# Kernel optimization log

Measured on AMD Instinct MI355X. Metric: run time of the kernel, lower is better.

The kernel has to match this reference:

```python
import math
import jax, jax.numpy as jnp
import numpy as np

G = 128        # graphs per batch
N0 = 512       # nodes per graph
H = 256        # hidden size
E = 524288     # edges (avg degree 8), intra-graph
RATIO = 0.8


def setup_inputs() -> dict:
    key = jax.random.key(0)
    ks = jax.random.split(key, 16)
    # intra-graph edges: E//G edges per graph
    eg = jnp.arange(E, dtype=jnp.int32) // (E // G)
    src = eg * N0 + jax.random.randint(ks[0], (E,), 0, N0, dtype=jnp.int32)
    dst = eg * N0 + jax.random.randint(ks[1], (E,), 0, N0, dtype=jnp.int32)
    s = 1.0 / math.sqrt(H)
    return {
        "x": jax.random.normal(ks[2], (G * N0, H), jnp.float32),
        "edge_src": src,
        "edge_dst": dst,
        "W_in": jax.random.normal(ks[3], (H, H), jnp.float32) * s,
        "b_in": jnp.zeros((H,), jnp.float32),
        "W_h0": jax.random.normal(ks[4], (H, H), jnp.float32) * s,
        "b_h0": jnp.zeros((H,), jnp.float32),
        "W_h1": jax.random.normal(ks[5], (H, H), jnp.float32) * s,
        "b_h1": jnp.zeros((H,), jnp.float32),
        "p_in": jax.random.normal(ks[6], (H,), jnp.float32),
        "p_h0": jax.random.normal(ks[7], (H,), jnp.float32),
        "p_h1": jax.random.normal(ks[8], (H,), jnp.float32),
        "att_w": jax.random.normal(ks[9], (H,), jnp.float32) * s,
        "att_b": jnp.zeros((1,), jnp.float32),
    }


def gcn_conv(x, W, b, src, dst, emask, num_nodes):
    # PyG GCNConv: lin -> sym-normalized propagate (with self loops, weight 1) -> bias
    h = x @ W
    deg = jax.ops.segment_sum(emask, dst, num_segments=num_nodes) + 1.0  # +1 self loop
    dis = jax.lax.rsqrt(deg)
    coef = dis[src] * dis[dst] * emask                    # [E]
    agg = jax.ops.segment_sum(h[src] * coef[:, None], dst, num_segments=num_nodes)
    agg = agg + h * (dis * dis)[:, None]                  # self-loop message
    return agg + b


def topk_pool(x, p, src, dst, emask, n_cur):
    # PyG TopKPooling: score = tanh(x.p/|p|), keep top ceil(ratio*n) per graph,
    # x' = x[perm]*score[perm], edges filtered to kept nodes and remapped.
    k = int(math.ceil(RATIO * n_cur))
    score = jnp.tanh((x @ p) / jnp.linalg.norm(p))        # [G*n_cur]
    _, idx = jax.lax.top_k(score.reshape(G, n_cur), k)    # [G,k]
    perm = (idx + (jnp.arange(G, dtype=idx.dtype) * n_cur)[:, None]).reshape(-1)
    x_new = x[perm] * score[perm][:, None]                # [G*k,H]
    mapping = jnp.full((G * n_cur,), -1, jnp.int32).at[perm].set(
        jnp.arange(G * k, dtype=jnp.int32))
    ns, nd = mapping[src], mapping[dst]
    valid = (ns >= 0) & (nd >= 0) & (emask > 0)
    return (x_new, jnp.where(valid, ns, 0), jnp.where(valid, nd, 0),
            valid.astype(x.dtype), k)


def att_pool(x, att_w, att_b, k):
    # GlobalAttention: per-graph softmax gate, weighted sum
    gate = (x @ att_w + att_b[0]).reshape(G, k)
    att = jax.nn.softmax(gate, axis=1)
    return jnp.einsum('gk,gkh->gh', att, x.reshape(G, k, H))


def reference(x, edge_src, edge_dst, W_in, b_in, W_h0, b_h0, W_h1, b_h1,
              p_in, p_h0, p_h1, att_w, att_b):
    src, dst = edge_src, edge_dst
    emask = jnp.ones((E,), x.dtype)
    n_cur = N0
    h = jax.nn.relu(gcn_conv(x, W_in, b_in, src, dst, emask, G * n_cur))
    h, src, dst, emask, n_cur = topk_pool(h, p_in, src, dst, emask, n_cur)
    out = att_pool(h, att_w, att_b, n_cur)
    for (W, b, p) in ((W_h0, b_h0, p_h0), (W_h1, b_h1, p_h1)):
        h = jax.nn.relu(gcn_conv(h, W, b, src, dst, emask, G * n_cur))
        h, src, dst, emask, n_cur = topk_pool(h, p, src, dst, emask, n_cur)
        out = out + att_pool(h, att_w, att_b, n_cur)
    return out  # [G, H]
```

## Files before the change

### kernel.cpp

```cpp
#include <hip/hip_runtime.h>
#include <cmath>

#define G_ 128
#define N0_ 512
#define H_ 256
#define E_ 524288
#define NODES0 (G_*N0_)

typedef _Float16 v8h __attribute__((ext_vector_type(8)));
typedef _Float16 v4h __attribute__((ext_vector_type(4)));
typedef float v4f __attribute__((ext_vector_type(4)));

#define TSTRIDE 72
#define TILEHW (128*TSTRIDE)

__device__ __forceinline__ void async_copy16(void* lds, const void* g) {
  __builtin_amdgcn_global_load_lds(
      (const __attribute__((address_space(1))) void*)g,
      (__attribute__((address_space(3))) void*)lds, 16, 0, 0);
}

__device__ __forceinline__ float4 f4fma(float4 a, float s, float4 acc) {
  acc.x = fmaf(a.x, s, acc.x); acc.y = fmaf(a.y, s, acc.y);
  acc.z = fmaf(a.z, s, acc.z); acc.w = fmaf(a.w, s, acc.w);
  return acc;
}

__device__ __forceinline__ float block_reduce_sum(float v, volatile float* red) {
  #pragma unroll
  for (int off = 32; off > 0; off >>= 1) v += __shfl_down(v, off);
  int lane = threadIdx.x & 63, wid = threadIdx.x >> 6;
  __syncthreads();
  if (lane == 0) red[wid] = v;
  __syncthreads();
  return red[0] + red[1] + red[2] + red[3];
}

__global__ __launch_bounds__(256) void pnorm_kernel(const float* __restrict__ p0,
                                                    const float* __restrict__ p1,
                                                    const float* __restrict__ p2,
                                                    float* __restrict__ pinv) {
  __shared__ float red[4];
  const float* p = (blockIdx.x == 0) ? p0 : (blockIdx.x == 1 ? p1 : p2);
  float v = p[threadIdx.x];
  float s = block_reduce_sum(v * v, red);
  if (threadIdx.x == 0) pinv[blockIdx.x] = 1.0f / sqrtf(s);
}

__global__ void init_kernel(int* __restrict__ cum, int* __restrict__ orig_of,
                            int* __restrict__ cnt, int n) {
  int v = blockIdx.x * 256 + threadIdx.x;
  if (v < n) { cum[v] = v; orig_of[v] = v; cnt[v] = 0; }
}

__global__ __launch_bounds__(256) void wconv_kernel(const float* __restrict__ W0,
                                                    const float* __restrict__ W1,
                                                    const float* __restrict__ W2,
                                                    _Float16* __restrict__ img) {
  int l = blockIdx.x >> 4;
  const float* W = (l == 0) ? W0 : (l == 1 ? W1 : W2);
  int bn = (blockIdx.x >> 3) & 1, kt = blockIdx.x & 7;
  int t = threadIdx.x;
  int n = t & 127, kh = t >> 7;
  int k0 = kt * 32 + kh * 16;
  _Float16* row = img + (size_t)l * 16 * TILEHW + ((size_t)(bn * 8 + kt) * 128 + n) * TSTRIDE;
  #pragma unroll
  for (int s = 0; s < 2; ++s) {
    v8h hv, lv;
    #pragma unroll
    for (int j = 0; j < 8; ++j) {
      float a = W[(size_t)(k0 + s * 8 + j) * 256 + bn * 128 + n];
      _Float16 h = (_Float16)a;
      hv[j] = h;
      lv[j] = (_Float16)(a - (float)h);
    }
    *(v8h*)&row[kh * 16 + s * 8] = hv;
    *(v8h*)&row[32 + kh * 16 + s * 8] = lv;
  }
}

__global__ void count0_kernel(const int* __restrict__ edst, int* __restrict__ cnt) {
  int e = blockIdx.x * 256 + threadIdx.x;
  if (e < E_) atomicAdd(&cnt[edst[e]], 1);
}

__global__ __launch_bounds__(256) void scan1_kernel(const int* __restrict__ cnt,
                                                    int* __restrict__ row0,
                                                    int* __restrict__ bsum,
                                                    float* __restrict__ dis,
                                                    int* __restrict__ cursor, int n) {
  __shared__ int sdata[256];
  int base = blockIdx.x * 1024;
  int t = threadIdx.x;
  int v[4]; int s = 0;
  #pragma unroll
  for (int i = 0; i < 4; ++i) {
    int idx = base + t * 4 + i;
    v[i] = (idx < n) ? cnt[idx] : 0;
    s += v[i];
    if (idx < n) {
      dis[idx] = 1.0f / sqrtf((float)v[i] + 1.0f);
      cursor[idx] = 0;
    }
  }
  sdata[t] = s;
  __syncthreads();
  for (int off = 1; off < 256; off <<= 1) {
    int x = (t >= off) ? sdata[t - off] : 0;
    __syncthreads();
    sdata[t] += x;
    __syncthreads();
  }
  int excl = sdata[t] - s;
  if (t == 255) bsum[blockIdx.x] = sdata[255];
  #pragma unroll
  for (int i = 0; i < 4; ++i) {
    int idx = base + t * 4 + i;
    if (idx < n) { row0[idx] = excl; excl += v[i]; }
  }
}

__global__ __launch_bounds__(256) void scan2_kernel(int* __restrict__ bsum,
                                                    int* __restrict__ row0, int nb, int n) {
  __shared__ int sdata[256];
  int t = threadIdx.x;
  int v = (t < nb) ? bsum[t] : 0;
  sdata[t] = v;
  __syncthreads();
  for (int off = 1; off < 256; off <<= 1) {
    int x = (t >= off) ? sdata[t - off] : 0;
    __syncthreads();
    sdata[t] += x;
    __syncthreads();
  }
  if (t < nb) bsum[t] = sdata[t] - v;
  if (t == 255) row0[n] = sdata[255];
}

__global__ void fill0_kernel(const int* __restrict__ esrc, const int* __restrict__ edst,
                             const int* __restrict__ row0, const int* __restrict__ bsum,
                             int* __restrict__ cursor, const float* __restrict__ dis,
                             int* __restrict__ csr0, int* __restrict__ csr_dst,
                             float* __restrict__ cf0) {
  int e = blockIdx.x * 256 + threadIdx.x;
  if (e >= E_) return;
  int d = edst[e], s = esrc[e];
  int pos = atomicAdd(&cursor[d], 1);
  int idx = row0[d] + bsum[d >> 10] + pos;
  csr0[idx] = s;
  csr_dst[idx] = d;
  cf0[idx] = dis[s] * dis[d];
}

__global__ void deg_kernel(const int* __restrict__ orig_of, const int* __restrict__ row0,
                           const int* __restrict__ bsum, const int* __restrict__ csr0,
                           const int* __restrict__ cum, float* __restrict__ dis, int nodes) {
  int v = blockIdx.x * 256 + threadIdx.x;
  if (v >= nodes) return;
  int o = orig_of[v];
  int rs = row0[o] + bsum[o >> 10];
  int o1 = o + 1;
  int re = row0[o1] + ((o1 < NODES0) ? bsum[o1 >> 10] : 0);
  int c = 0;
  for (int j = rs; j < re; ++j) c += (cum[csr0[j]] >= 0) ? 1 : 0;
  dis[v] = rsqrtf((float)c + 1.0f);
}

__global__ void remap_kernel(const int* __restrict__ csr0, const int* __restrict__ csr_dst,
                             const int* __restrict__ cum, const float* __restrict__ dis,
                             int* __restrict__ src_l, float* __restrict__ cf_l) {
  int j = blockIdx.x * 256 + threadIdx.x;
  if (j >= E_) return;
  int md = cum[csr_dst[j]];
  if (md < 0) return;
  int ms = cum[csr0[j]];
  src_l[j] = (ms >= 0) ? ms : 0;
  cf_l[j] = (ms >= 0) ? dis[ms] * dis[md] : 0.0f;
}

__global__ __launch_bounds__(256) void gemm_f16x3_kernel(const float* __restrict__ A,
                                                         const int* __restrict__ perm,
                                                         const float* __restrict__ score,
                                                         const _Float16* __restrict__ Wimg,
                                                         float* __restrict__ C) {
  __shared__ _Float16 As[TILEHW];
  __shared__ _Float16 Ws[TILEHW];
  const int tid = threadIdx.x;
  const int bm = blockIdx.x >> 1;
  const int bn = blockIdx.x & 1;
  const int lane = tid & 63, wid = tid >> 6;
  const int wm = wid >> 1, wn = wid & 1;
  const int l15 = lane & 15, kg = lane >> 4;

  v4f acc[4][4];
  #pragma unroll
  for (int i = 0; i < 4; ++i)
    #pragma unroll
    for (int j = 0; j < 4; ++j) acc[i][j] = (v4f){0.f, 0.f, 0.f, 0.f};

  int arow[4], acc4[4];
  const float* aptr[4];
  float ascale[4];
  #pragma unroll
  for (int i = 0; i < 4; ++i) {
    int c = tid + 256 * i;
    arow[i] = c >> 3;
    acc4[i] = c & 7;
    int R = bm * 128 + arow[i];
    int pr = perm ? perm[R] : R;
    ascale[i] = perm ? score[pr] : 1.0f;
    aptr[i] = A + (size_t)pr * 256 + acc4[i] * 4;
  }
  const _Float16* wtile0 = Wimg + (size_t)bn * 8 * TILEHW;

  float4 pa[4];
  #pragma unroll
  for (int i = 0; i < 4; ++i) pa[i] = *(const float4*)(aptr[i] + 0);

  for (int kt = 0; kt < 8; ++kt) {
    {
      const _Float16* wt = wtile0 + (size_t)kt * TILEHW;
      for (int cb = wid; cb < 18; cb += 4)
        async_copy16(&Ws[cb * 512], wt + (size_t)cb * 512 + lane * 8);
    }
    #pragma unroll
    for (int i = 0; i < 4; ++i) {
      float av[4] = {pa[i].x * ascale[i], pa[i].y * ascale[i],
                     pa[i].z * ascale[i], pa[i].w * ascale[i]};
      v4h hv, lv;
      #pragma unroll
      for (int j = 0; j < 4; ++j) {
        _Float16 h = (_Float16)av[j];
        hv[j] = h;
        lv[j] = (_Float16)(av[j] - (float)h);
      }
      _Float16* dst = &As[arow[i] * TSTRIDE + acc4[i] * 4];
      *(v4h*)(dst) = hv;
      *(v4h*)(dst + 32) = lv;
    }
    __syncthreads();

    if (kt < 7) {
      #pragma unroll
      for (int i = 0; i < 4; ++i)
        pa[i] = *(const float4*)(aptr[i] + (kt + 1) * 32);
    }

    v8h ah[4], bh[4], al[4], bl[4];
    #pragma unroll
    for (int i = 0; i < 4; ++i)
      ah[i] = *(const v8h*)&As[(wm * 64 + i * 16 + l15) * TSTRIDE + kg * 8];
    #pragma unroll
    for (int j = 0; j < 4; ++j)
      bh[j] = *(const v8h*)&Ws[(wn * 64 + j * 16 + l15) * TSTRIDE + kg * 8];
    #pragma unroll
    for (int i = 0; i < 4; ++i)
      #pragma unroll
      for (int j = 0; j < 4; ++j)
        acc[i][j] = __builtin_amdgcn_mfma_f32_16x16x32_f16(ah[i], bh[j], acc[i][j], 0, 0, 0);
    #pragma unroll
    for (int i = 0; i < 4; ++i)
      al[i] = *(const v8h*)&As[(wm * 64 + i * 16 + l15) * TSTRIDE + 32 + kg * 8];
    #pragma unroll
    for (int i = 0; i < 4; ++i)
      #pragma unroll
      for (int j = 0; j < 4; ++j)
        acc[i][j] = __builtin_amdgcn_mfma_f32_16x16x32_f16(al[i], bh[j], acc[i][j], 0, 0, 0);
    #pragma unroll
    for (int j = 0; j < 4; ++j)
      bl[j] = *(const v8h*)&Ws[(wn * 64 + j * 16 + l15) * TSTRIDE + 32 + kg * 8];
    #pragma unroll
    for (int i = 0; i < 4; ++i)
      #pragma unroll
      for (int j = 0; j < 4; ++j)
        acc[i][j] = __builtin_amdgcn_mfma_f32_16x16x32_f16(ah[i], bl[j], acc[i][j], 0, 0, 0);
    __syncthreads();
  }

  #pragma unroll
  for (int i = 0; i < 4; ++i) {
    #pragma unroll
    for (int j = 0; j < 4; ++j) {
      #pragma unroll
      for (int r = 0; r < 4; ++r) {
        int row = bm * 128 + wm * 64 + i * 16 + kg * 4 + r;
        int col = bn * 128 + wn * 64 + j * 16 + l15;
        C[(size_t)row * 256 + col] = acc[i][j][r];
      }
    }
  }
}

__global__ __launch_bounds__(256) void agg_score_kernel(
    const float4* __restrict__ hlin4, const float* __restrict__ dis,
    const float4* __restrict__ bias4,
    const int* __restrict__ orig_of, const int* __restrict__ row0,
    const int* __restrict__ bsum,
    const int* __restrict__ src_arr, const float* __restrict__ cf_arr,
    const float4* __restrict__ p4, const float* __restrict__ pinvp,
    float4* __restrict__ hout4, float* __restrict__ score, int q) {
  int blk = (blockIdx.x & 7) * q + (blockIdx.x >> 3);
  int wave = threadIdx.x >> 6, lane = threadIdx.x & 63;
  int v = blk * 4 + wave;
  float dv = dis[v];
  float self = dv * dv;
  float4 h = hlin4[(size_t)v * 64 + lane];
  float4 acc = make_float4(h.x * self, h.y * self, h.z * self, h.w * self);
  int o = orig_of[v];
  int rs = row0[o] + bsum[o >> 10];
  int o1 = o + 1;
  int re = row0[o1] + ((o1 < NODES0) ? bsum[o1 >> 10] : 0);
  int j = rs;
  for (; j + 8 <= re; j += 8) {
    int s[8]; float c[8]; float4 hh[8];
    #pragma unroll
    for (int u = 0; u < 8; ++u) { s[u] = src_arr[j + u]; c[u] = cf_arr[j + u]; }
    #pragma unroll
    for (int u = 0; u < 8; ++u) hh[u] = hlin4[(size_t)s[u] * 64 + lane];
    #pragma unroll
    for (int u = 0; u < 8; ++u) acc = f4fma(hh[u], c[u], acc);
  }
  if (j + 4 <= re) {
    int s[4]; float c[4]; float4 hh[4];
    #pragma unroll
    for (int u = 0; u < 4; ++u) { s[u] = src_arr[j + u]; c[u] = cf_arr[j + u]; }
    #pragma unroll
    for (int u = 0; u < 4; ++u) hh[u] = hlin4[(size_t)s[u] * 64 + lane];
    #pragma unroll
    for (int u = 0; u < 4; ++u) acc = f4fma(hh[u], c[u], acc);
    j += 4;
  }
  for (; j < re; ++j) {
    acc = f4fma(hlin4[(size_t)src_arr[j] * 64 + lane], cf_arr[j], acc);
  }
  float4 b = bias4[lane];
  acc.x = fmaxf(acc.x + b.x, 0.0f); acc.y = fmaxf(acc.y + b.y, 0.0f);
  acc.z = fmaxf(acc.z + b.z, 0.0f); acc.w = fmaxf(acc.w + b.w, 0.0f);
  hout4[(size_t)v * 64 + lane] = acc;
  float4 pv = p4[lane];
  float s = acc.x * pv.x + acc.y * pv.y + acc.z * pv.z + acc.w * pv.w;
  #pragma unroll
  for (int off = 32; off > 0; off >>= 1) s += __shfl_down(s, off);
  if (lane == 0) score[v] = tanhf(s * pinvp[0]);
}

__global__ __launch_bounds__(256) void topk_kernel(const float* __restrict__ score, int n, int k,
                                                   int* __restrict__ cum,
                                                   const int* __restrict__ orig_prev,
                                                   int* __restrict__ orig_new,
                                                   int* __restrict__ perm) {
  __shared__ float key[512];
  __shared__ int kid[512];
  __shared__ int newmap[512];
  int g = blockIdx.x, t = threadIdx.x;
  for (int i = t; i < 512; i += 256) {
    key[i] = (i < n) ? score[(size_t)g * n + i] : -INFINITY;
    kid[i] = i;
    if (i < n) newmap[i] = -1;
  }
  __syncthreads();
  for (int kk = 2; kk <= 512; kk <<= 1) {
    for (int j = kk >> 1; j > 0; j >>= 1) {
      #pragma unroll
      for (int half = 0; half < 2; ++half) {
        int i = t + half * 256;
        int ixj = i ^ j;
        if (ixj > i) {
          float ka = key[i]; int ia = kid[i];
          float kb = key[ixj]; int ib = kid[ixj];
          bool b_first = (kb > ka) || (kb == ka && ib < ia);
          bool sw = ((i & kk) == 0) ? b_first : !b_first;
          if (sw) { key[i] = kb; kid[i] = ib; key[ixj] = ka; kid[ixj] = ia; }
        }
      }
      __syncthreads();
    }
  }
  for (int i = t; i < k; i += 256) {
    int local = kid[i];
    perm[g * k + i] = g * n + local;
    newmap[local] = g * k + i;
    orig_new[g * k + i] = orig_prev[g * n + local];
  }
  __syncthreads();
  #pragma unroll
  for (int u = 0; u < N0_ / 256; ++u) {
    int v = g * N0_ + u * 256 + t;
    int c = cum[v];
    if (c >= 0) cum[v] = newmap[c - g * n];
  }
}

__global__ __launch_bounds__(512) void pool_kernel(
    const float4* __restrict__ h4, const float* __restrict__ score,
    const int* __restrict__ perm,
    const float4* __restrict__ attw4, const float* __restrict__ attb,
    float* __restrict__ out, int k, int add) {
  __shared__ float wmax[8], wsum[8];
  __shared__ float4 waccs[8][64];
  int g = blockIdx.x, t = threadIdx.x;
  int wave = t >> 6, lane = t & 63;
  float4 aw = attw4[lane];
  float ab = attb[0];

  float m = -INFINITY, ssum = 0.0f;
  float4 acc = make_float4(0.f, 0.f, 0.f, 0.f);
  for (int i = wave; i < k; i += 8) {
    int s = perm[g * k + i];
    float sc = score[s];
    float4 hv = h4[(size_t)s * 64 + lane];
    float4 val = make_float4(hv.x * sc, hv.y * sc, hv.z * sc, hv.w * sc);
    float gd = val.x * aw.x + val.y * aw.y + val.z * aw.z + val.w * aw.w;
    #pragma unroll
    for (int off = 32; off > 0; off >>= 1) gd += __shfl_xor(gd, off);
    float gi = gd + ab;
    float mnew = fmaxf(m, gi);
    float f = __expf(m - mnew);
    float e = __expf(gi - mnew);
    acc.x = acc.x * f + val.x * e; acc.y = acc.y * f + val.y * e;
    acc.z = acc.z * f + val.z * e; acc.w = acc.w * f + val.w * e;
    ssum = ssum * f + e;
    m = mnew;
  }
  if (lane == 0) { wmax[wave] = m; wsum[wave] = ssum; }
  waccs[wave][lane] = acc;
  __syncthreads();
  if (wave == 0) {
    float mstar = wmax[0];
    #pragma unroll
    for (int w = 1; w < 8; ++w) mstar = fmaxf(mstar, wmax[w]);
    float stot = 0.0f;
    float4 a = make_float4(0.f, 0.f, 0.f, 0.f);
    #pragma unroll
    for (int w = 0; w < 8; ++w) {
      float sc = __expf(wmax[w] - mstar);
      stot += wsum[w] * sc;
      float4 wa = waccs[w][lane];
      a.x += wa.x * sc; a.y += wa.y * sc; a.z += wa.z * sc; a.w += wa.w * sc;
    }
    float inv = 1.0f / stot;
    a.x *= inv; a.y *= inv; a.z *= inv; a.w *= inv;
    float4* o4 = (float4*)out + (size_t)g * 64 + lane;
    if (add) {
      float4 prev = *o4;
      a.x += prev.x; a.y += prev.y; a.z += prev.z; a.w += prev.w;
    }
    *o4 = a;
  }
}

extern "C" void kernel_launch(void* const* d_in, const int* in_sizes, int n_in,
                              void* d_out, int out_size, void* d_ws, size_t ws_size,
                              hipStream_t stream) {
  const float* x    = (const float*)d_in[0];
  const int*   esrc = (const int*)d_in[1];
  const int*   edst = (const int*)d_in[2];
  const float* Wl[3] = {(const float*)d_in[3], (const float*)d_in[5], (const float*)d_in[7]};
  const float* bl[3] = {(const float*)d_in[4], (const float*)d_in[6], (const float*)d_in[8]};
  const float* pl[3] = {(const float*)d_in[9], (const float*)d_in[10], (const float*)d_in[11]};
  const float* attw = (const float*)d_in[12];
  const float* attb = (const float*)d_in[13];
  float* out = (float*)d_out;

  char* w = (char*)d_ws;
  auto carve = [&](size_t bytes) { char* p = w; w += (bytes + 255) & ~(size_t)255; return p; };
  float* bufA    = (float*)carve((size_t)NODES0 * H_ * 4);
  float* bufB    = (float*)carve((size_t)NODES0 * H_ * 4);
  int*   csr0    = (int*)  carve((size_t)E_ * 4);
  int*   csr_dst = (int*)  carve((size_t)E_ * 4);
  float* cf0     = (float*)carve((size_t)E_ * 4);
  int*   src_l   = (int*)  carve((size_t)E_ * 4);
  float* cf_l    = (float*)carve((size_t)E_ * 4);
  int*   cnt     = (int*)  carve((size_t)NODES0 * 4);
  int*   row0    = (int*)  carve((size_t)(NODES0 + 1) * 4);
  int*   cursor  = (int*)  carve((size_t)NODES0 * 4);
  float* dis     = (float*)carve((size_t)NODES0 * 4);
  float* score   = (float*)carve((size_t)NODES0 * 4);
  int*   cum_map = (int*)  carve((size_t)NODES0 * 4);
  int*   origA   = (int*)  carve((size_t)NODES0 * 4);
  int*   origB   = (int*)  carve((size_t)NODES0 * 4);
  int*   perm    = (int*)  carve((size_t)NODES0 * 4);
  int*   bsum    = (int*)  carve(256 * 4);
  float* pinv    = (float*)carve(16);
  _Float16* Wimg = (_Float16*)carve((size_t)3 * 16 * TILEHW * 2);
  (void)ws_size; (void)in_sizes; (void)n_in; (void)out_size;

  pnorm_kernel<<<3, 256, 0, stream>>>(pl[0], pl[1], pl[2], pinv);
  init_kernel<<<NODES0 / 256, 256, 0, stream>>>(cum_map, origA, cnt, NODES0);
  wconv_kernel<<<48, 256, 0, stream>>>(Wl[0], Wl[1], Wl[2], Wimg);

  count0_kernel<<<E_ / 256, 256, 0, stream>>>(edst, cnt);
  int nb0 = (NODES0 + 1023) / 1024;
  scan1_kernel<<<nb0, 256, 0, stream>>>(cnt, row0, bsum, dis, cursor, NODES0);
  scan2_kernel<<<1, 256, 0, stream>>>(bsum, row0, nb0, NODES0);
  fill0_kernel<<<E_ / 256, 256, 0, stream>>>(esrc, edst, row0, bsum, cursor, dis,
                                             csr0, csr_dst, cf0);

  int n_cur = N0_;
  int* origs[2] = {origA, origB};
  for (int l = 0; l < 3; ++l) {
    int nodes = G_ * n_cur;
    int* orig_cur = origs[l & 1];
    int* orig_nxt = origs[(l & 1) ^ 1];

    if (l > 0) {
      deg_kernel<<<(nodes + 255) / 256, 256, 0, stream>>>(orig_cur, row0, bsum, csr0,
                                                          cum_map, dis, nodes);
      remap_kernel<<<E_ / 256, 256, 0, stream>>>(csr0, csr_dst, cum_map, dis, src_l, cf_l);
    }

    gemm_f16x3_kernel<<<(nodes / 128) * 2, 256, 0, stream>>>(
        (l == 0) ? x : bufB, (l == 0) ? nullptr : perm, score,
        Wimg + (size_t)l * 16 * TILEHW, bufA);

    int agg_blocks = nodes / 4;
    agg_score_kernel<<<agg_blocks, 256, 0, stream>>>(
        (const float4*)bufA, dis, (const float4*)bl[l], orig_cur, row0, bsum,
        (l == 0) ? csr0 : src_l, (l == 0) ? cf0 : cf_l,
        (const float4*)pl[l], pinv + l, (float4*)bufB, score, agg_blocks / 8);

    int kk = (int)std::ceil(0.8 * (double)n_cur);
    topk_kernel<<<G_, 256, 0, stream>>>(score, n_cur, kk, cum_map, orig_cur, orig_nxt, perm);

    pool_kernel<<<G_, 512, 0, stream>>>(
        (const float4*)bufB, score, perm, (const float4*)attw, attb, out, kk, l > 0 ? 1 : 0);

    n_cur = kk;
  }
}
```

Baseline: 411.2 us.

## Stage per-graph feature slices in LDS for GCN aggregation, split score reduction

The aggregation kernel now runs one 1024-thread block per graph per pair of 64-column slices. It stages the graph's node features for each slice into LDS with async global-to-LDS copies, then gathers neighbours from LDS instead of global memory, relying on edges being intra-graph. Per-slice partial score dots go to a new buffer, and the topk kernel sums them and applies tanh. This cuts scattered global gathers but uses only 256 blocks with 128KB LDS each, which limits occupancy and parallelism. Invalid edges now point at the destination node so LDS indices stay in range.

```diff
diff --git a/kernel.cpp b/kernel.cpp
--- a/kernel.cpp
+++ b/kernel.cpp
@@ -174,7 +174,7 @@
   int md = cum[csr_dst[j]];
   if (md < 0) return;
   int ms = cum[csr0[j]];
-  src_l[j] = (ms >= 0) ? ms : 0;
+  src_l[j] = (ms >= 0) ? ms : md;
   cf_l[j] = (ms >= 0) ? dis[ms] * dis[md] : 0.0f;
 }
 
@@ -291,60 +291,66 @@
   }
 }
 
-__global__ __launch_bounds__(256) void agg_score_kernel(
-    const float4* __restrict__ hlin4, const float* __restrict__ dis,
-    const float4* __restrict__ bias4,
+__global__ __launch_bounds__(1024) void agg_score_kernel(
+    const float* __restrict__ hlin, const float* __restrict__ dis,
+    const float* __restrict__ bias,
     const int* __restrict__ orig_of, const int* __restrict__ row0,
     const int* __restrict__ bsum,
     const int* __restrict__ src_arr, const float* __restrict__ cf_arr,
-    const float4* __restrict__ p4, const float* __restrict__ pinvp,
-    float4* __restrict__ hout4, float* __restrict__ score, int q) {
-  int blk = (blockIdx.x & 7) * q + (blockIdx.x >> 3);
-  int wave = threadIdx.x >> 6, lane = threadIdx.x & 63;
-  int v = blk * 4 + wave;
-  float dv = dis[v];
-  float self = dv * dv;
-  float4 h = hlin4[(size_t)v * 64 + lane];
-  float4 acc = make_float4(h.x * self, h.y * self, h.z * self, h.w * self);
-  int o = orig_of[v];
-  int rs = row0[o] + bsum[o >> 10];
-  int o1 = o + 1;
-  int re = row0[o1] + ((o1 < NODES0) ? bsum[o1 >> 10] : 0);
-  int j = rs;
-  for (; j + 8 <= re; j += 8) {
-    int s[8]; float c[8]; float4 hh[8];
-    #pragma unroll
-    for (int u = 0; u < 8; ++u) { s[u] = src_arr[j + u]; c[u] = cf_arr[j + u]; }
-    #pragma unroll
-    for (int u = 0; u < 8; ++u) hh[u] = hlin4[(size_t)s[u] * 64 + lane];
-    #pragma unroll
-    for (int u = 0; u < 8; ++u) acc = f4fma(hh[u], c[u], acc);
-  }
-  if (j + 4 <= re) {
-    int s[4]; float c[4]; float4 hh[4];
-    #pragma unroll
-    for (int u = 0; u < 4; ++u) { s[u] = src_arr[j + u]; c[u] = cf_arr[j + u]; }
-    #pragma unroll
-    for (int u = 0; u < 4; ++u) hh[u] = hlin4[(size_t)s[u] * 64 + lane];
-    #pragma unroll
-    for (int u = 0; u < 4; ++u) acc = f4fma(hh[u], c[u], acc);
-    j += 4;
-  }
-  for (; j < re; ++j) {
-    acc = f4fma(hlin4[(size_t)src_arr[j] * 64 + lane], cf_arr[j], acc);
-  }
-  float4 b = bias4[lane];
-  acc.x = fmaxf(acc.x + b.x, 0.0f); acc.y = fmaxf(acc.y + b.y, 0.0f);
-  acc.z = fmaxf(acc.z + b.z, 0.0f); acc.w = fmaxf(acc.w + b.w, 0.0f);
-  hout4[(size_t)v * 64 + lane] = acc;
-  float4 pv = p4[lane];
-  float s = acc.x * pv.x + acc.y * pv.y + acc.z * pv.z + acc.w * pv.w;
-  #pragma unroll
-  for (int off = 32; off > 0; off >>= 1) s += __shfl_down(s, off);
-  if (lane == 0) score[v] = tanhf(s * pinvp[0]);
-}
-
-__global__ __launch_bounds__(256) void topk_kernel(const float* __restrict__ score, int n, int k,
+    const float* __restrict__ p,
+    float* __restrict__ hout, float* __restrict__ scorepart, int n) {
+  __shared__ float sh[512 * 64];
+  int g = blockIdx.x >> 1;
+  int s0 = (blockIdx.x & 1) * 2;
+  int t = threadIdx.x, wave = t >> 6, lane = t & 63;
+  const int nodebase = g * n;
+
+  for (int s = s0; s < s0 + 2; ++s) {
+    for (int r4 = wave * 4; r4 < n; r4 += 64) {
+      const float* src = hlin + (size_t)(nodebase + r4 + (lane >> 4)) * 256
+                              + s * 64 + (lane & 15) * 4;
+      async_copy16(&sh[r4 * 64], src);
+    }
+    __syncthreads();
+
+    float bb = bias[s * 64 + lane];
+    float pp = p[s * 64 + lane];
+
+    for (int vl = wave; vl < n; vl += 16) {
+      int v = nodebase + vl;
+      float dv = dis[v];
+      float acc = sh[vl * 64 + lane] * (dv * dv);
+      int o = orig_of[v];
+      int rs = row0[o] + bsum[o >> 10];
+      int o1 = o + 1;
+      int re = row0[o1] + ((o1 < NODES0) ? bsum[o1 >> 10] : 0);
+      int j = rs;
+      for (; j + 8 <= re; j += 8) {
+        int sl[8]; float cf[8];
+        #pragma unroll
+        for (int u = 0; u < 8; ++u) { sl[u] = src_arr[j + u] - nodebase; cf[u] = cf_arr[j + u]; }
+        float hv[8];
+        #pragma unroll
+        for (int u = 0; u < 8; ++u) hv[u] = sh[sl[u] * 64 + lane];
+        #pragma unroll
+        for (int u = 0; u < 8; ++u) acc = fmaf(hv[u], cf[u], acc);
+      }
+      for (; j < re; ++j)
+        acc = fmaf(sh[(src_arr[j] - nodebase) * 64 + lane], cf_arr[j], acc);
+      acc = fmaxf(acc + bb, 0.0f);
+      hout[(size_t)v * 256 + s * 64 + lane] = acc;
+      float sdot = acc * pp;
+      #pragma unroll
+      for (int off = 32; off > 0; off >>= 1) sdot += __shfl_down(sdot, off);
+      if (lane == 0) scorepart[(size_t)v * 4 + s] = sdot;
+    }
+    __syncthreads();
+  }
+}
+
+__global__ __launch_bounds__(256) void topk_kernel(const float* __restrict__ scorepart,
+                                                   const float* __restrict__ pinvp,
+                                                   float* __restrict__ score, int n, int k,
                                                    int* __restrict__ cum,
                                                    const int* __restrict__ orig_prev,
                                                    int* __restrict__ orig_new,
@@ -353,10 +359,18 @@
   __shared__ int kid[512];
   __shared__ int newmap[512];
   int g = blockIdx.x, t = threadIdx.x;
+  float pinv = pinvp[0];
   for (int i = t; i < 512; i += 256) {
-    key[i] = (i < n) ? score[(size_t)g * n + i] : -INFINITY;
+    float sc = -INFINITY;
+    if (i < n) {
+      const float* sp = scorepart + (size_t)(g * n + i) * 4;
+      float tot = ((sp[0] + sp[1]) + sp[2]) + sp[3];
+      sc = tanhf(tot * pinv);
+      score[g * n + i] = sc;
+      newmap[i] = -1;
+    }
+    key[i] = sc;
     kid[i] = i;
-    if (i < n) newmap[i] = -1;
   }
   __syncthreads();
   for (int kk = 2; kk <= 512; kk <<= 1) {
@@ -476,6 +490,7 @@
   int*   cursor  = (int*)  carve((size_t)NODES0 * 4);
   float* dis     = (float*)carve((size_t)NODES0 * 4);
   float* score   = (float*)carve((size_t)NODES0 * 4);
+  float* spart   = (float*)carve((size_t)NODES0 * 4 * 4);
   int*   cum_map = (int*)  carve((size_t)NODES0 * 4);
   int*   origA   = (int*)  carve((size_t)NODES0 * 4);
   int*   origB   = (int*)  carve((size_t)NODES0 * 4);
@@ -513,14 +528,14 @@
         (l == 0) ? x : bufB, (l == 0) ? nullptr : perm, score,
         Wimg + (size_t)l * 16 * TILEHW, bufA);
 
-    int agg_blocks = nodes / 4;
-    agg_score_kernel<<<agg_blocks, 256, 0, stream>>>(
-        (const float4*)bufA, dis, (const float4*)bl[l], orig_cur, row0, bsum,
+    agg_score_kernel<<<G_ * 2, 1024, 0, stream>>>(
+        bufA, dis, bl[l], orig_cur, row0, bsum,
         (l == 0) ? csr0 : src_l, (l == 0) ? cf0 : cf_l,
-        (const float4*)pl[l], pinv + l, (float4*)bufB, score, agg_blocks / 8);
+        pl[l], bufB, spart, n_cur);
 
     int kk = (int)std::ceil(0.8 * (double)n_cur);
-    topk_kernel<<<G_, 256, 0, stream>>>(score, n_cur, kk, cum_map, orig_cur, orig_nxt, perm);
+    topk_kernel<<<G_, 256, 0, stream>>>(spart, pinv + l, score, n_cur, kk,
+                                        cum_map, orig_cur, orig_nxt, perm);
 
     pool_kernel<<<G_, 512, 0, stream>>>(
         (const float4*)bufB, score, perm, (const float4*)attw, attb, out, kk, l > 0 ? 1 : 0);
```

Measured after the change: 602.2 us. 1.46x slower.

## Fuse top-k with attention pooling and pack edge src/coef into int2

Applied to the files above, without the earlier changes.

Merges the top-k sort kernel and the attention pooling kernel into one 512-thread kernel per graph. The pooling step now reads sorted scores and indices straight from shared memory instead of indirecting through perm and the global score array. Edge source indices and normalization coefficients are interleaved into int2 pairs, so the aggregation loop does one 8-byte load per edge instead of two scattered 4-byte loads. The sorted scores are also written to a compact sscore array so the GEMM gather reads them contiguously. Invalid remapped edges now point at the destination node with zero coefficient rather than node 0.

```diff
diff --git a/kernel.cpp b/kernel.cpp
--- a/kernel.cpp
+++ b/kernel.cpp
@@ -141,7 +141,7 @@
                              const int* __restrict__ row0, const int* __restrict__ bsum,
                              int* __restrict__ cursor, const float* __restrict__ dis,
                              int* __restrict__ csr0, int* __restrict__ csr_dst,
-                             float* __restrict__ cf0) {
+                             int2* __restrict__ pair0) {
   int e = blockIdx.x * 256 + threadIdx.x;
   if (e >= E_) return;
   int d = edst[e], s = esrc[e];
@@ -149,7 +149,7 @@
   int idx = row0[d] + bsum[d >> 10] + pos;
   csr0[idx] = s;
   csr_dst[idx] = d;
-  cf0[idx] = dis[s] * dis[d];
+  pair0[idx] = make_int2(s, __float_as_int(dis[s] * dis[d]));
 }
 
 __global__ void deg_kernel(const int* __restrict__ orig_of, const int* __restrict__ row0,
@@ -168,19 +168,19 @@
 
 __global__ void remap_kernel(const int* __restrict__ csr0, const int* __restrict__ csr_dst,
                              const int* __restrict__ cum, const float* __restrict__ dis,
-                             int* __restrict__ src_l, float* __restrict__ cf_l) {
+                             int2* __restrict__ pair_l) {
   int j = blockIdx.x * 256 + threadIdx.x;
   if (j >= E_) return;
   int md = cum[csr_dst[j]];
   if (md < 0) return;
   int ms = cum[csr0[j]];
-  src_l[j] = (ms >= 0) ? ms : 0;
-  cf_l[j] = (ms >= 0) ? dis[ms] * dis[md] : 0.0f;
+  pair_l[j] = make_int2((ms >= 0) ? ms : md,
+                        __float_as_int((ms >= 0) ? dis[ms] * dis[md] : 0.0f));
 }
 
 __global__ __launch_bounds__(256) void gemm_f16x3_kernel(const float* __restrict__ A,
                                                          const int* __restrict__ perm,
-                                                         const float* __restrict__ score,
+                                                         const float* __restrict__ sscore,
                                                          const _Float16* __restrict__ Wimg,
                                                          float* __restrict__ C) {
   __shared__ _Float16 As[TILEHW];
@@ -208,7 +208,7 @@
     acc4[i] = c & 7;
     int R = bm * 128 + arow[i];
     int pr = perm ? perm[R] : R;
-    ascale[i] = perm ? score[pr] : 1.0f;
+    ascale[i] = perm ? sscore[R] : 1.0f;
     aptr[i] = A + (size_t)pr * 256 + acc4[i] * 4;
   }
   const _Float16* wtile0 = Wimg + (size_t)bn * 8 * TILEHW;
@@ -296,7 +296,7 @@
     const float4* __restrict__ bias4,
     const int* __restrict__ orig_of, const int* __restrict__ row0,
     const int* __restrict__ bsum,
-    const int* __restrict__ src_arr, const float* __restrict__ cf_arr,
+    const int2* __restrict__ edge,
     const float4* __restrict__ p4, const float* __restrict__ pinvp,
     float4* __restrict__ hout4, float* __restrict__ score, int q) {
   int blk = (blockIdx.x & 7) * q + (blockIdx.x >> 3);
@@ -314,7 +314,10 @@
   for (; j + 8 <= re; j += 8) {
     int s[8]; float c[8]; float4 hh[8];
     #pragma unroll
-    for (int u = 0; u < 8; ++u) { s[u] = src_arr[j + u]; c[u] = cf_arr[j + u]; }
+    for (int u = 0; u < 8; ++u) {
+      int2 e = edge[j + u];
+      s[u] = e.x; c[u] = __int_as_float(e.y);
+    }
     #pragma unroll
     for (int u = 0; u < 8; ++u) hh[u] = hlin4[(size_t)s[u] * 64 + lane];
     #pragma unroll
@@ -323,7 +326,10 @@
   if (j + 4 <= re) {
     int s[4]; float c[4]; float4 hh[4];
     #pragma unroll
-    for (int u = 0; u < 4; ++u) { s[u] = src_arr[j + u]; c[u] = cf_arr[j + u]; }
+    for (int u = 0; u < 4; ++u) {
+      int2 e = edge[j + u];
+      s[u] = e.x; c[u] = __int_as_float(e.y);
+    }
     #pragma unroll
     for (int u = 0; u < 4; ++u) hh[u] = hlin4[(size_t)s[u] * 64 + lane];
     #pragma unroll
@@ -331,7 +337,8 @@
     j += 4;
   }
   for (; j < re; ++j) {
-    acc = f4fma(hlin4[(size_t)src_arr[j] * 64 + lane], cf_arr[j], acc);
+    int2 e = edge[j];
+    acc = f4fma(hlin4[(size_t)e.x * 64 + lane], __int_as_float(e.y), acc);
   }
   float4 b = bias4[lane];
   acc.x = fmaxf(acc.x + b.x, 0.0f); acc.y = fmaxf(acc.y + b.y, 0.0f);
@@ -344,71 +351,59 @@
   if (lane == 0) score[v] = tanhf(s * pinvp[0]);
 }
 
-__global__ __launch_bounds__(256) void topk_kernel(const float* __restrict__ score, int n, int k,
-                                                   int* __restrict__ cum,
-                                                   const int* __restrict__ orig_prev,
-                                                   int* __restrict__ orig_new,
-                                                   int* __restrict__ perm) {
+__global__ __launch_bounds__(512) void topk_pool_kernel(
+    const float* __restrict__ score, int n, int k,
+    int* __restrict__ cum, const int* __restrict__ orig_prev,
+    int* __restrict__ orig_new, int* __restrict__ perm, float* __restrict__ sscore,
+    const float4* __restrict__ h4, const float4* __restrict__ attw4,
+    const float* __restrict__ attb, float* __restrict__ out, int add) {
   __shared__ float key[512];
   __shared__ int kid[512];
   __shared__ int newmap[512];
-  int g = blockIdx.x, t = threadIdx.x;
-  for (int i = t; i < 512; i += 256) {
-    key[i] = (i < n) ? score[(size_t)g * n + i] : -INFINITY;
-    kid[i] = i;
-    if (i < n) newmap[i] = -1;
-  }
-  __syncthreads();
-  for (int kk = 2; kk <= 512; kk <<= 1) {
-    for (int j = kk >> 1; j > 0; j >>= 1) {
-      #pragma unroll
-      for (int half = 0; half < 2; ++half) {
-        int i = t + half * 256;
-        int ixj = i ^ j;
-        if (ixj > i) {
-          float ka = key[i]; int ia = kid[i];
-          float kb = key[ixj]; int ib = kid[ixj];
-          bool b_first = (kb > ka) || (kb == ka && ib < ia);
-          bool sw = ((i & kk) == 0) ? b_first : !b_first;
-          if (sw) { key[i] = kb; kid[i] = ib; key[ixj] = ka; kid[ixj] = ia; }
-        }
-      }
-      __syncthreads();
-    }
-  }
-  for (int i = t; i < k; i += 256) {
-    int local = kid[i];
-    perm[g * k + i] = g * n + local;
-    newmap[local] = g * k + i;
-    orig_new[g * k + i] = orig_prev[g * n + local];
-  }
-  __syncthreads();
-  #pragma unroll
-  for (int u = 0; u < N0_ / 256; ++u) {
-    int v = g * N0_ + u * 256 + t;
-    int c = cum[v];
-    if (c >= 0) cum[v] = newmap[c - g * n];
-  }
-}
-
-__global__ __launch_bounds__(512) void pool_kernel(
-    const float4* __restrict__ h4, const float* __restrict__ score,
-    const int* __restrict__ perm,
-    const float4* __restrict__ attw4, const float* __restrict__ attb,
-    float* __restrict__ out, int k, int add) {
   __shared__ float wmax[8], wsum[8];
   __shared__ float4 waccs[8][64];
   int g = blockIdx.x, t = threadIdx.x;
+
+  key[t] = (t < n) ? score[(size_t)g * n + t] : -INFINITY;
+  kid[t] = t;
+  if (t < n) newmap[t] = -1;
+  __syncthreads();
+  for (int kk = 2; kk <= 512; kk <<= 1) {
+    for (int j = kk >> 1; j > 0; j >>= 1) {
+      int i = t, ixj = i ^ j;
+      if (ixj > i) {
+        float ka = key[i]; int ia = kid[i];
+        float kb = key[ixj]; int ib = kid[ixj];
+        bool b_first = (kb > ka) || (kb == ka && ib < ia);
+        bool sw = ((i & kk) == 0) ? b_first : !b_first;
+        if (sw) { key[i] = kb; kid[i] = ib; key[ixj] = ka; kid[ixj] = ia; }
+      }
+      __syncthreads();
+    }
+  }
+  if (t < k) {
+    int local = kid[t];
+    perm[g * k + t] = g * n + local;
+    newmap[local] = g * k + t;
+    orig_new[g * k + t] = orig_prev[g * n + local];
+    sscore[g * k + t] = key[t];
+  }
+  __syncthreads();
+  {
+    int v = g * N0_ + t;
+    int c = cum[v];
+    if (c >= 0) cum[v] = newmap[c - g * n];
+  }
+
   int wave = t >> 6, lane = t & 63;
   float4 aw = attw4[lane];
   float ab = attb[0];
-
   float m = -INFINITY, ssum = 0.0f;
   float4 acc = make_float4(0.f, 0.f, 0.f, 0.f);
   for (int i = wave; i < k; i += 8) {
-    int s = perm[g * k + i];
-    float sc = score[s];
-    float4 hv = h4[(size_t)s * 64 + lane];
+    int node = g * n + kid[i];
+    float sc = key[i];
+    float4 hv = h4[(size_t)node * 64 + lane];
     float4 val = make_float4(hv.x * sc, hv.y * sc, hv.z * sc, hv.w * sc);
     float gd = val.x * aw.x + val.y * aw.y + val.z * aw.z + val.w * aw.w;
     #pragma unroll
@@ -468,14 +463,14 @@
   float* bufB    = (float*)carve((size_t)NODES0 * H_ * 4);
   int*   csr0    = (int*)  carve((size_t)E_ * 4);
   int*   csr_dst = (int*)  carve((size_t)E_ * 4);
-  float* cf0     = (float*)carve((size_t)E_ * 4);
-  int*   src_l   = (int*)  carve((size_t)E_ * 4);
-  float* cf_l    = (float*)carve((size_t)E_ * 4);
+  int2*  pair0   = (int2*) carve((size_t)E_ * 8);
+  int2*  pair_l  = (int2*) carve((size_t)E_ * 8);
   int*   cnt     = (int*)  carve((size_t)NODES0 * 4);
   int*   row0    = (int*)  carve((size_t)(NODES0 + 1) * 4);
   int*   cursor  = (int*)  carve((size_t)NODES0 * 4);
   float* dis     = (float*)carve((size_t)NODES0 * 4);
   float* score   = (float*)carve((size_t)NODES0 * 4);
+  float* sscore  = (float*)carve((size_t)NODES0 * 4);
   int*   cum_map = (int*)  carve((size_t)NODES0 * 4);
   int*   origA   = (int*)  carve((size_t)NODES0 * 4);
   int*   origB   = (int*)  carve((size_t)NODES0 * 4);
@@ -494,7 +489,7 @@
   scan1_kernel<<<nb0, 256, 0, stream>>>(cnt, row0, bsum, dis, cursor, NODES0);
   scan2_kernel<<<1, 256, 0, stream>>>(bsum, row0, nb0, NODES0);
   fill0_kernel<<<E_ / 256, 256, 0, stream>>>(esrc, edst, row0, bsum, cursor, dis,
-                                             csr0, csr_dst, cf0);
+                                             csr0, csr_dst, pair0);
 
   int n_cur = N0_;
   int* origs[2] = {origA, origB};
@@ -506,24 +501,23 @@
     if (l > 0) {
       deg_kernel<<<(nodes + 255) / 256, 256, 0, stream>>>(orig_cur, row0, bsum, csr0,
                                                           cum_map, dis, nodes);
-      remap_kernel<<<E_ / 256, 256, 0, stream>>>(csr0, csr_dst, cum_map, dis, src_l, cf_l);
+      remap_kernel<<<E_ / 256, 256, 0, stream>>>(csr0, csr_dst, cum_map, dis, pair_l);
     }
 
     gemm_f16x3_kernel<<<(nodes / 128) * 2, 256, 0, stream>>>(
-        (l == 0) ? x : bufB, (l == 0) ? nullptr : perm, score,
+        (l == 0) ? x : bufB, (l == 0) ? nullptr : perm, sscore,
         Wimg + (size_t)l * 16 * TILEHW, bufA);
 
     int agg_blocks = nodes / 4;
     agg_score_kernel<<<agg_blocks, 256, 0, stream>>>(
         (const float4*)bufA, dis, (const float4*)bl[l], orig_cur, row0, bsum,
-        (l == 0) ? csr0 : src_l, (l == 0) ? cf0 : cf_l,
+        (l == 0) ? pair0 : pair_l,
         (const float4*)pl[l], pinv + l, (float4*)bufB, score, agg_blocks / 8);
 
     int kk = (int)std::ceil(0.8 * (double)n_cur);
-    topk_kernel<<<G_, 256, 0, stream>>>(score, n_cur, kk, cum_map, orig_cur, orig_nxt, perm);
-
-    pool_kernel<<<G_, 512, 0, stream>>>(
-        (const float4*)bufB, score, perm, (const float4*)attw, attb, out, kk, l > 0 ? 1 : 0);
+    topk_pool_kernel<<<G_, 512, 0, stream>>>(
+        score, n_cur, kk, cum_map, orig_cur, orig_nxt, perm, sscore,
+        (const float4*)bufB, (const float4*)attw, attb, out, l > 0 ? 1 : 0);
 
     n_cur = kk;
   }
```

Measured after the change: 386.2 us. 6.1% less time.
